# Kernel optimization log

Hardware: AMD Instinct MI355X
Metric: run time of the kernel (lower is better)

Reference implementation:

```python
import jax, jax.numpy as jnp
import numpy as np

N, D, F_IN, F_MID, F_OUT = 200000, 3, 128, 512, 128


def setup_inputs() -> dict:
    key = jax.random.key(0)
    ks = jax.random.split(key, 6)
    s = lambda fan_in: 1.0 / np.sqrt(fan_in)
    return {
        "x": jax.random.normal(ks[0], (N, D, F_IN), dtype=jnp.float32),
        "W_prop": jax.random.normal(ks[1], (F_IN, F_OUT), dtype=jnp.float32) * s(F_IN),
        "W1": jax.random.normal(ks[2], (F_IN, F_MID), dtype=jnp.float32) * s(F_IN),
        "b1": jax.random.normal(ks[3], (F_MID,), dtype=jnp.float32) * s(F_IN),
        "W2": jax.random.normal(ks[4], (F_MID, F_OUT), dtype=jnp.float32) * s(F_MID),
        "b2": jax.random.normal(ks[5], (F_OUT,), dtype=jnp.float32) * s(F_MID),
    }


def reference(x, W_prop, W1, b1, W2, b2):
    # linear_weight (Proportional): bias-free linear on the feature axis,
    # applied to the rank-1 equivariant tensor -> stays equivariant.
    linear_x = jnp.einsum("ndf,fg->ndg", x, W_prop)  # [N, D, F_OUT]
    # contraction(x): invariant inner product over spatial components.
    c = jnp.einsum("ndf,ndf->nf", x, x)  # [N, F_IN]
    # norm_function = identity; MLP chain: Linear->tanh->Linear->identity
    h = jnp.tanh(c @ W1 + b1)  # [N, F_MID]
    h = h @ W2 + b2            # [N, F_OUT]
    # tensor_product(rank-1, rank-0): broadcast multiply over spatial dim.
    return linear_x * h[:, None, :]  # [N, D, F_OUT]
```

## Files before the change

kernel.cpp:

```cpp
#include <hip/hip_runtime.h>
#include <hip/hip_bf16.h>

#define NROWS   200000
#define TILE    32
#define NBLOCKS (NROWS / TILE)

typedef __attribute__((ext_vector_type(4))) float f32x4;
typedef __attribute__((ext_vector_type(8))) short bf16x8;

__device__ __forceinline__ unsigned pk2(float lo, float hi) {
  float2 f{lo, hi};
  __hip_bfloat162 h = __float22bfloat162_rn(f);
  unsigned u;
  __builtin_memcpy(&u, &h, 4);
  return u;
}
__device__ __forceinline__ unsigned short bf1(float v) {
  return (unsigned short)pk2(v, v);
}
__device__ __forceinline__ unsigned short f2bf(float f) {
  unsigned b = __float_as_uint(f);
  b += 0x7fffu + ((b >> 16) & 1u);
  return (unsigned short)(b >> 16);
}
__device__ __forceinline__ float bflo(unsigned pk) { return __uint_as_float(pk << 16); }
__device__ __forceinline__ float bfhi(unsigned pk) { return __uint_as_float(pk & 0xffff0000u); }
__device__ __forceinline__ f32x4 mfma16(bf16x8 a, bf16x8 b, f32x4 c) {
  return __builtin_amdgcn_mfma_f32_16x16x32_bf16(a, b, c, 0, 0, 0);
}
__device__ __forceinline__ float fast_tanh(float x) {
  float e = __expf(2.0f * x);
  return 1.0f - __fdividef(2.0f, e + 1.0f);
}
__device__ __forceinline__ int SW (int b) { return b ^ (((b >> 8) & 7) << 4); }
__device__ __forceinline__ int SW2(int b) { return b ^ (((b >> 9) & 7) << 4); }

__global__ void prep_weights(const float* __restrict__ Wp,
                             const float* __restrict__ W1,
                             const float* __restrict__ W2,
                             unsigned short* __restrict__ wpf,
                             unsigned short* __restrict__ w1f,
                             unsigned short* __restrict__ w2f) {
  int t = blockIdx.x * 256 + threadIdx.x;
  int q = t >> 6, l = t & 63;
  const float* W; unsigned short* dst; int NT, Nout, qb; bool inter;
  if (q < 32)       { W = Wp; dst = wpf; NT = 8;  Nout = 128; qb = q;       inter = true;  }
  else if (q < 160) { W = W1; dst = w1f; NT = 32; Nout = 512; qb = q - 32;  inter = true;  }
  else              { W = W2; dst = w2f; NT = 8;  Nout = 128; qb = q - 160; inter = false; }
  int kt = qb / NT, nt = qb % NT;
  int row0 = kt * 32 + 8 * (l >> 4);
  int col  = inter ? (nt >> 1) * 32 + 2 * (l & 15) + (nt & 1)
                   : nt * 16 + (l & 15);
  unsigned short v[8];
#pragma unroll
  for (int i = 0; i < 8; ++i) v[i] = f2bf(W[(row0 + i) * Nout + col]);
  uint4 pack;
  pack.x = (unsigned)v[0] | ((unsigned)v[1] << 16);
  pack.y = (unsigned)v[2] | ((unsigned)v[3] << 16);
  pack.z = (unsigned)v[4] | ((unsigned)v[5] << 16);
  pack.w = (unsigned)v[6] | ((unsigned)v[7] << 16);
  *(uint4*)(dst + (size_t)(qb * 64 + l) * 8) = pack;
}

__global__ __launch_bounds__(512, 6) void fused_kernel(
    const float* __restrict__ x,
    const float* __restrict__ b1,
    const float* __restrict__ b2,
    const unsigned short* __restrict__ wpf,
    const unsigned short* __restrict__ w1f,
    const unsigned short* __restrict__ w2f,
    float* __restrict__ out) {
  __shared__ __align__(16) char smem[49152];
  const int t = threadIdx.x;
  const int l = t & 63;
  const int w = t >> 6;
  const int lr = l & 15;
  const int lq = l >> 4;
  const int p = w & 3;
  const int h = w >> 2;
  const long n0 = (long)blockIdx.x * TILE;

#pragma unroll
  for (int k = 0; k < 2; ++k) {
    int pc = t + k * 512, r = pc >> 5, f = (pc & 31) * 4;
    const float* xp = x + (n0 + r) * 384 + f;
    float4 a = *(const float4*)(xp);
    float4 b = *(const float4*)(xp + 128);
    float4 c = *(const float4*)(xp + 256);
    uint2 s0 = { pk2(a.x, a.y), pk2(a.z, a.w) };
    uint2 s1 = { pk2(b.x, b.y), pk2(b.z, b.w) };
    uint2 s2 = { pk2(c.x, c.y), pk2(c.z, c.w) };
    uint2 sc = { pk2(a.x*a.x + b.x*b.x + c.x*c.x,
                     a.y*a.y + b.y*b.y + c.y*c.y),
                 pk2(a.z*a.z + b.z*b.z + c.z*c.z,
                     a.w*a.w + b.w*b.w + c.w*c.w) };
    *(uint2*)(smem + SW((3 * r + 0) * 256 + f * 2)) = s0;
    *(uint2*)(smem + SW((3 * r + 1) * 256 + f * 2)) = s1;
    *(uint2*)(smem + SW((3 * r + 2) * 256 + f * 2)) = s2;
    *(uint2*)(smem + SW(32768 + r * 256 + f * 2))   = sc;
  }
  __syncthreads();

  unsigned lx[3][4];
  {
    f32x4 acc1[3][2] = {};
#pragma unroll
    for (int kt = 0; kt < 4; ++kt) {
      bf16x8 a[3];
#pragma unroll
      for (int m = 0; m < 3; ++m)
        a[m] = *(const bf16x8*)(smem + SW((h * 48 + m * 16 + lr) * 256 + kt * 64 + lq * 16));
#pragma unroll
      for (int jj = 0; jj < 2; ++jj) {
        bf16x8 b = *(const bf16x8*)(wpf + (size_t)((kt * 8 + 2 * p + jj) * 64 + l) * 8);
#pragma unroll
        for (int m = 0; m < 3; ++m) acc1[m][jj] = mfma16(a[m], b, acc1[m][jj]);
      }
    }
#pragma unroll
    for (int m = 0; m < 3; ++m)
#pragma unroll
      for (int reg = 0; reg < 4; ++reg)
        lx[m][reg] = pk2(acc1[m][0][reg], acc1[m][1][reg]);
  }

  f32x4 acc2[2][2];
  auto do_gemm2 = [&](int ch) {
#pragma unroll
    for (int m = 0; m < 2; ++m)
#pragma unroll
      for (int jj = 0; jj < 2; ++jj) { f32x4 z = {}; acc2[m][jj] = z; }
#pragma unroll
    for (int kt = 0; kt < 4; ++kt) {
      bf16x8 a2[2];
#pragma unroll
      for (int m = 0; m < 2; ++m)
        a2[m] = *(const bf16x8*)(smem + SW(32768 + (m * 16 + lr) * 256 + kt * 64 + lq * 16));
#pragma unroll
      for (int jj = 0; jj < 2; ++jj) {
        bf16x8 b = *(const bf16x8*)(w1f + (size_t)((kt * 32 + ch * 16 + 2 * w + jj) * 64 + l) * 8);
#pragma unroll
        for (int m = 0; m < 2; ++m) acc2[m][jj] = mfma16(a2[m], b, acc2[m][jj]);
      }
    }
  };
  auto do_epi = [&](int ch) {
    const int bufb = ch * 16384;
    float2 b1v = *(const float2*)(b1 + ch * 256 + w * 32 + 2 * lr);
#pragma unroll
    for (int m = 0; m < 2; ++m)
#pragma unroll
      for (int reg = 0; reg < 4; ++reg) {
        int row = m * 16 + 4 * lq + reg;
        unsigned pk = pk2(fast_tanh(acc2[m][0][reg] + b1v.x),
                          fast_tanh(acc2[m][1][reg] + b1v.y));
        *(unsigned*)(smem + SW2(bufb + row * 512 + w * 64 + 4 * lr)) = pk;
      }
  };
  f32x4 acc3[2] = {};
  auto do_gemm3 = [&](int ch) {
    const int bufb = ch * 16384;
#pragma unroll
    for (int kt = 0; kt < 8; ++kt) {
      bf16x8 b = *(const bf16x8*)(w2f + (size_t)(((ch * 8 + kt) * 8 + w) * 64 + l) * 8);
#pragma unroll
      for (int m = 0; m < 2; ++m) {
        bf16x8 a3 = *(const bf16x8*)(smem + SW2(bufb + (m * 16 + lr) * 512 + kt * 64 + lq * 16));
        acc3[m] = mfma16(a3, b, acc3[m]);
      }
    }
  };

  do_gemm2(0);
  __syncthreads();

  do_epi(0);
  do_gemm2(1);
  __syncthreads();

  do_gemm3(0);
  do_epi(1);
  __syncthreads();

  do_gemm3(1);

  {
    float b2v = b2[w * 16 + lr];
#pragma unroll
    for (int m = 0; m < 2; ++m)
#pragma unroll
      for (int reg = 0; reg < 4; ++reg) {
        int row = m * 16 + 4 * lq + reg;
        *(unsigned short*)(smem + SW(40960 + row * 256 + (w * 16 + lr) * 2)) =
            bf1(acc3[m][reg] + b2v);
      }
  }
  __syncthreads();

#pragma unroll
  for (int m = 0; m < 3; ++m)
#pragma unroll
    for (int reg = 0; reg < 4; ++reg) {
      int rp = h * 48 + m * 16 + 4 * lq + reg;
      int n = rp / 3;
      unsigned hp = *(const unsigned*)(smem + SW(40960 + n * 256 + p * 64 + 4 * lr));
      unsigned pk = lx[m][reg];
      float2 o = { bflo(pk) * bflo(hp), bfhi(pk) * bfhi(hp) };
      *(float2*)(out + n0 * 384 + (long)rp * 128 + p * 32 + 2 * lr) = o;
    }
}

extern "C" void kernel_launch(void* const* d_in, const int* in_sizes, int n_in,
                              void* d_out, int out_size, void* d_ws, size_t ws_size,
                              hipStream_t stream) {
  const float* x  = (const float*)d_in[0];
  const float* Wp = (const float*)d_in[1];
  const float* W1 = (const float*)d_in[2];
  const float* b1 = (const float*)d_in[3];
  const float* W2 = (const float*)d_in[4];
  const float* b2 = (const float*)d_in[5];
  float* out = (float*)d_out;

  if (ws_size < 294912) return;
  unsigned short* w1f = (unsigned short*)d_ws;
  unsigned short* w2f = (unsigned short*)((char*)d_ws + 131072);
  unsigned short* wpf = (unsigned short*)((char*)d_ws + 262144);

  prep_weights<<<72, 256, 0, stream>>>(Wp, W1, W2, wpf, w1f, w2f);
  fused_kernel<<<NBLOCKS, 512, 0, stream>>>(x, b1, b2, wpf, w1f, w2f, out);
}
```

Baseline: 230.4 us.

## Split hidden layer into four 128-wide chunks to shrink LDS footprint

Processes the 512-wide hidden layer in four chunks of 128 instead of two of 256, using two 8 KB ping-pong buffers. It also re-splits the first MLP GEMM so each wave covers 16 rows by 32 columns per chunk. This cuts shared memory per block from 48 KB to 32 KB, which may let more blocks reside per CU. In exchange it adds two more block-wide barriers and shorter GEMM phases with less overlap per phase.

```diff
diff --git a/kernel.cpp b/kernel.cpp
--- a/kernel.cpp
+++ b/kernel.cpp
@@ -33,7 +33,6 @@
   return 1.0f - __fdividef(2.0f, e + 1.0f);
 }
 __device__ __forceinline__ int SW (int b) { return b ^ (((b >> 8) & 7) << 4); }
-__device__ __forceinline__ int SW2(int b) { return b ^ (((b >> 9) & 7) << 4); }
 
 __global__ void prep_weights(const float* __restrict__ Wp,
                              const float* __restrict__ W1,
@@ -70,7 +69,7 @@
     const unsigned short* __restrict__ w1f,
     const unsigned short* __restrict__ w2f,
     float* __restrict__ out) {
-  __shared__ __align__(16) char smem[49152];
+  __shared__ __align__(16) char smem[32768];
   const int t = threadIdx.x;
   const int l = t & 63;
   const int w = t >> 6;
@@ -97,7 +96,7 @@
     *(uint2*)(smem + SW((3 * r + 0) * 256 + f * 2)) = s0;
     *(uint2*)(smem + SW((3 * r + 1) * 256 + f * 2)) = s1;
     *(uint2*)(smem + SW((3 * r + 2) * 256 + f * 2)) = s2;
-    *(uint2*)(smem + SW(32768 + r * 256 + f * 2))   = sc;
+    *(uint2*)(smem + SW(24576 + r * 256 + f * 2))   = sc;
   }
   __syncthreads();
 
@@ -124,48 +123,39 @@
         lx[m][reg] = pk2(acc1[m][0][reg], acc1[m][1][reg]);
   }
 
-  f32x4 acc2[2][2];
+  f32x4 acc2[2];
   auto do_gemm2 = [&](int ch) {
-#pragma unroll
-    for (int m = 0; m < 2; ++m)
-#pragma unroll
-      for (int jj = 0; jj < 2; ++jj) { f32x4 z = {}; acc2[m][jj] = z; }
+    { f32x4 z = {}; acc2[0] = z; acc2[1] = z; }
 #pragma unroll
     for (int kt = 0; kt < 4; ++kt) {
-      bf16x8 a2[2];
-#pragma unroll
-      for (int m = 0; m < 2; ++m)
-        a2[m] = *(const bf16x8*)(smem + SW(32768 + (m * 16 + lr) * 256 + kt * 64 + lq * 16));
+      bf16x8 a2 = *(const bf16x8*)(smem + SW(24576 + (h * 16 + lr) * 256 + kt * 64 + lq * 16));
 #pragma unroll
       for (int jj = 0; jj < 2; ++jj) {
-        bf16x8 b = *(const bf16x8*)(w1f + (size_t)((kt * 32 + ch * 16 + 2 * w + jj) * 64 + l) * 8);
-#pragma unroll
-        for (int m = 0; m < 2; ++m) acc2[m][jj] = mfma16(a2[m], b, acc2[m][jj]);
+        bf16x8 b = *(const bf16x8*)(w1f + (size_t)((kt * 32 + ch * 8 + 2 * p + jj) * 64 + l) * 8);
+        acc2[jj] = mfma16(a2, b, acc2[jj]);
       }
     }
   };
   auto do_epi = [&](int ch) {
-    const int bufb = ch * 16384;
-    float2 b1v = *(const float2*)(b1 + ch * 256 + w * 32 + 2 * lr);
-#pragma unroll
-    for (int m = 0; m < 2; ++m)
-#pragma unroll
-      for (int reg = 0; reg < 4; ++reg) {
-        int row = m * 16 + 4 * lq + reg;
-        unsigned pk = pk2(fast_tanh(acc2[m][0][reg] + b1v.x),
-                          fast_tanh(acc2[m][1][reg] + b1v.y));
-        *(unsigned*)(smem + SW2(bufb + row * 512 + w * 64 + 4 * lr)) = pk;
-      }
+    const int bufb = (ch & 1) * 8192;
+    float2 b1v = *(const float2*)(b1 + ch * 128 + p * 32 + 2 * lr);
+#pragma unroll
+    for (int reg = 0; reg < 4; ++reg) {
+      int row = h * 16 + 4 * lq + reg;
+      unsigned pk = pk2(fast_tanh(acc2[0][reg] + b1v.x),
+                        fast_tanh(acc2[1][reg] + b1v.y));
+      *(unsigned*)(smem + SW(bufb + row * 256 + p * 64 + 4 * lr)) = pk;
+    }
   };
   f32x4 acc3[2] = {};
   auto do_gemm3 = [&](int ch) {
-    const int bufb = ch * 16384;
-#pragma unroll
-    for (int kt = 0; kt < 8; ++kt) {
-      bf16x8 b = *(const bf16x8*)(w2f + (size_t)(((ch * 8 + kt) * 8 + w) * 64 + l) * 8);
+    const int bufb = (ch & 1) * 8192;
+#pragma unroll
+    for (int kt = 0; kt < 4; ++kt) {
+      bf16x8 b = *(const bf16x8*)(w2f + (size_t)(((ch * 4 + kt) * 8 + w) * 64 + l) * 8);
 #pragma unroll
       for (int m = 0; m < 2; ++m) {
-        bf16x8 a3 = *(const bf16x8*)(smem + SW2(bufb + (m * 16 + lr) * 512 + kt * 64 + lq * 16));
+        bf16x8 a3 = *(const bf16x8*)(smem + SW(bufb + (m * 16 + lr) * 256 + kt * 64 + lq * 16));
         acc3[m] = mfma16(a3, b, acc3[m]);
       }
     }
@@ -180,9 +170,19 @@
 
   do_gemm3(0);
   do_epi(1);
+  do_gemm2(2);
   __syncthreads();
 
   do_gemm3(1);
+  do_epi(2);
+  do_gemm2(3);
+  __syncthreads();
+
+  do_gemm3(2);
+  do_epi(3);
+  __syncthreads();
+
+  do_gemm3(3);
 
   {
     float b2v = b2[w * 16 + lr];
@@ -191,7 +191,7 @@
 #pragma unroll
       for (int reg = 0; reg < 4; ++reg) {
         int row = m * 16 + 4 * lq + reg;
-        *(unsigned short*)(smem + SW(40960 + row * 256 + (w * 16 + lr) * 2)) =
+        *(unsigned short*)(smem + SW(16384 + row * 256 + (w * 16 + lr) * 2)) =
             bf1(acc3[m][reg] + b2v);
       }
   }
@@ -203,7 +203,7 @@
     for (int reg = 0; reg < 4; ++reg) {
       int rp = h * 48 + m * 16 + 4 * lq + reg;
       int n = rp / 3;
-      unsigned hp = *(const unsigned*)(smem + SW(40960 + n * 256 + p * 64 + 4 * lr));
+      unsigned hp = *(const unsigned*)(smem + SW(16384 + n * 256 + p * 64 + 4 * lr));
       unsigned pk = lx[m][reg];
       float2 o = { bflo(pk) * bflo(hp), bfhi(pk) * bfhi(hp) };
       *(float2*)(out + n0 * 384 + (long)rp * 128 + p * 32 + 2 * lr) = o;
```

After: 278.3 us. 20.8% more time.
